# Performance work log

Measured on AMD Instinct MI355X. Metric: run time of the kernel, lower is better.

## Reference

```python
import jax, jax.numpy as jnp
import numpy as np

B, N, M, C, DIN, DIM, SDIM = 4, 65536, 32768, 4, 64, 64, 32


def setup_inputs() -> dict:
    key = jax.random.key(0)
    ks = jax.random.split(key, 8)
    return {
        "last": jax.random.normal(ks[0], (B, N, C, DIN), jnp.float32),
        "sample": jax.random.normal(ks[1], (B, N, C, SDIM), jnp.float32),
        "child_l": jax.random.randint(ks[2], (M,), 0, N),
        "child_r": jax.random.randint(ks[3], (M,), 0, N),
        "child_s": jax.random.randint(ks[4], (M,), 0, N),
        "W_merge": jax.random.normal(ks[5], (2 * DIN, DIM), jnp.float32) / np.float32(np.sqrt(2 * DIN)),
        "b_merge": jnp.zeros((DIM,), jnp.float32),
        "a_merge": jnp.full((1,), 0.25, jnp.float32),
        "W_ms": jax.random.normal(ks[6], (C * SDIM, C * DIM), jnp.float32) / np.float32(np.sqrt(C * SDIM)),
        "b_ms": jnp.zeros((C * DIM,), jnp.float32),
        "a_ms": jnp.full((1,), 0.25, jnp.float32),
        "W_msamp": jax.random.normal(ks[7], (2 * DIM, DIM), jnp.float32) / np.float32(np.sqrt(2 * DIM)),
        "b_msamp": jnp.zeros((DIM,), jnp.float32),
        "a_msamp": jnp.full((1,), 0.25, jnp.float32),
    }


def _prelu(x, a):
    return jnp.where(x >= 0, x, a * x)


def reference(last, sample, child_l, child_r, child_s,
              W_merge, b_merge, a_merge,
              W_ms, b_ms, a_ms,
              W_msamp, b_msamp, a_msamp):
    # gather left/right child embeddings: [B, M, C, DIN] each
    lch = last[:, child_l]
    rch = last[:, child_r]
    x = jnp.concatenate([lch, rch], axis=-1)           # [B, M, C, 2*DIN]
    ans = _prelu(x @ W_merge + b_merge, a_merge)       # [B, M, C, DIM]

    # sampled branch: gather + flatten channel*sample_dim, FC to channel*dim
    s = sample[:, child_s]                             # [B, M, C, SDIM]
    s = s.reshape(s.shape[0], s.shape[1], -1)          # [B, M, C*SDIM]
    s = _prelu(s @ W_ms + b_ms, a_ms)                  # [B, M, C*DIM]
    s = s.reshape(s.shape[0], s.shape[1], ans.shape[2], -1)  # [B, M, C, DIM]

    y = jnp.concatenate([ans, s], axis=-1)             # [B, M, C, 2*DIM]
    out = _prelu(y @ W_msamp + b_msamp, a_msamp)       # [B, M, C, DIM]
    # dropout is identity in eval mode
    return out
```

## Files before the change

### kernel.cpp

```cpp
#include <hip/hip_runtime.h>
#include <hip/hip_bf16.h>

#define B_    4
#define N_TOT 65536
#define M_TOT 32768
#define C_    4
#define DIN_  64
#define DIM_  64
#define SDIM_ 32

typedef __bf16 bf16x8 __attribute__((ext_vector_type(8)));
typedef float  f32x4  __attribute__((ext_vector_type(4)));
typedef bf16x8 bf16x8_a __attribute__((may_alias));
typedef uint2  uint2_a  __attribute__((may_alias));

__device__ __forceinline__ float prelu_f(float x, float a) { return x >= 0.0f ? x : a * x; }

__global__ void prep_weights(const float* __restrict__ Wm,
                             const float* __restrict__ Wms,
                             const float* __restrict__ Wsa,
                             __hip_bfloat16* __restrict__ ws)
{
    int t = blockIdx.x * blockDim.x + threadIdx.x;
    if (t < 8192) {
        int n = t >> 7, k = t & 127;
        ws[t] = __float2bfloat16(Wm[k * 64 + n]);
    } else if (t < 40960) {
        int u = t - 8192; int n = u >> 7, k = u & 127;
        ws[t] = __float2bfloat16(Wms[k * 256 + n]);
    } else if (t < 49152) {
        int u = t - 40960; int n = u >> 7, k = u & 127;
        ws[t] = __float2bfloat16(Wsa[k * 64 + n]);
    }
}

__global__ __launch_bounds__(256, 2) void encoder_fused(
    const float* __restrict__ last,
    const float* __restrict__ sample,
    const int* __restrict__ child_l,
    const int* __restrict__ child_r,
    const int* __restrict__ child_s,
    const __bf16* __restrict__ wt,
    const float* __restrict__ b_merge, const float* __restrict__ a_merge_p,
    const float* __restrict__ b_ms,    const float* __restrict__ a_ms_p,
    const float* __restrict__ b_msamp, const float* __restrict__ a_msamp_p,
    float* __restrict__ out)
{
    __shared__ char lds_raw[4][16384];
    const int tid  = threadIdx.x;
    const int lane = tid & 63;
    const int wid  = tid >> 6;
    char* Y = &lds_raw[wid][0];

    const int group  = blockIdx.x * 4 + wid;
    const int b      = group >> 11;
    const int m_base = (group & 2047) << 4;

    const int g   = lane >> 4;
    const int j15 = lane & 15;

    const float a_merge = *a_merge_p;
    const float a_ms    = *a_ms_p;
    const float a_msamp = *a_msamp_p;

    const __bf16* Wm_t  = wt;
    const __bf16* Wms_t = wt + 8192;
    const __bf16* Wsa_t = wt + 40960;

    bf16x8 wm[4][4];
    f32x4  bm[4];
#pragma unroll
    for (int n = 0; n < 4; ++n) {
        bm[n] = *(const f32x4*)(b_merge + n * 16 + g * 4);
#pragma unroll
        for (int kk = 0; kk < 4; ++kk)
            wm[n][kk] = *(const bf16x8*)(Wm_t + (n * 16 + j15) * 128 + kk * 32 + g * 8);
    }

#pragma unroll
    for (int t = 0; t < 4; ++t) {
        const int node_local = t * 4 + (j15 >> 2);
        const int c  = j15 & 3;
        const int m  = m_base + node_local;
        const int cl = child_l[m];
        const int cr = child_r[m];
        const float* lsrc = last + ((size_t)(b * N_TOT + cl) * C_ + c) * DIN_;
        const float* rsrc = last + ((size_t)(b * N_TOT + cr) * C_ + c) * DIN_;

        bf16x8 xf[4];
#pragma unroll
        for (int kk = 0; kk < 4; ++kk) {
            const int k = kk * 32 + g * 8;
            const float* src = (k < 64) ? (lsrc + k) : (rsrc + (k - 64));
            f32x4 f0 = *(const f32x4*)(src);
            f32x4 f1 = *(const f32x4*)(src + 4);
            bf16x8 v;
            v[0] = (__bf16)f0[0]; v[1] = (__bf16)f0[1]; v[2] = (__bf16)f0[2]; v[3] = (__bf16)f0[3];
            v[4] = (__bf16)f1[0]; v[5] = (__bf16)f1[1]; v[6] = (__bf16)f1[2]; v[7] = (__bf16)f1[3];
            xf[kk] = v;
        }

        const int row = t * 16 + j15;
        const int swz = (row & 7) << 4;
#pragma unroll
        for (int n = 0; n < 4; ++n) {
            f32x4 acc = {0.f, 0.f, 0.f, 0.f};
#pragma unroll
            for (int kk = 0; kk < 4; ++kk)
                acc = __builtin_amdgcn_mfma_f32_16x16x32_bf16(wm[n][kk], xf[kk], acc, 0, 0, 0);
            union { __bf16 h[4]; uint2 u2; } p;
#pragma unroll
            for (int r = 0; r < 4; ++r)
                p.h[r] = (__bf16)prelu_f(acc[r] + bm[n][r], a_merge);
            const int byte = row * 256 + ((n * 32 + g * 8) ^ swz);
            *(uint2_a*)(Y + byte) = p.u2;
        }
    }

    {
        const int m  = m_base + j15;
        const int cs = child_s[m];
        const float* ssrc = sample + (size_t)(b * N_TOT + cs) * 128;
        bf16x8 sf[4];
#pragma unroll
        for (int kk = 0; kk < 4; ++kk) {
            const int k = kk * 32 + g * 8;
            f32x4 f0 = *(const f32x4*)(ssrc + k);
            f32x4 f1 = *(const f32x4*)(ssrc + k + 4);
            bf16x8 v;
            v[0] = (__bf16)f0[0]; v[1] = (__bf16)f0[1]; v[2] = (__bf16)f0[2]; v[3] = (__bf16)f0[3];
            v[4] = (__bf16)f1[0]; v[5] = (__bf16)f1[1]; v[6] = (__bf16)f1[2]; v[7] = (__bf16)f1[3];
            sf[kk] = v;
        }
#pragma unroll
        for (int n2 = 0; n2 < 16; ++n2) {
            f32x4 acc = {0.f, 0.f, 0.f, 0.f};
#pragma unroll
            for (int kk = 0; kk < 4; ++kk) {
                bf16x8 w = *(const bf16x8*)(Wms_t + (n2 * 16 + j15) * 128 + kk * 32 + g * 8);
                acc = __builtin_amdgcn_mfma_f32_16x16x32_bf16(w, sf[kk], acc, 0, 0, 0);
            }
            f32x4 bb = *(const f32x4*)(b_ms + n2 * 16 + g * 4);
            const int f0i = n2 * 16 + g * 4;
            const int row = j15 * 4 + (f0i >> 6);
            const int byte = row * 256 + ((128 + (f0i & 63) * 2) ^ ((row & 7) << 4));
            union { __bf16 h[4]; uint2 u2; } p;
#pragma unroll
            for (int r = 0; r < 4; ++r)
                p.h[r] = (__bf16)prelu_f(acc[r] + bb[r], a_ms);
            *(uint2_a*)(Y + byte) = p.u2;
        }
    }

    bf16x8 wa[4][4];
    f32x4  ba[4];
#pragma unroll
    for (int n = 0; n < 4; ++n) {
        ba[n] = *(const f32x4*)(b_msamp + n * 16 + g * 4);
#pragma unroll
        for (int kk = 0; kk < 4; ++kk)
            wa[n][kk] = *(const bf16x8*)(Wsa_t + (n * 16 + j15) * 128 + kk * 32 + g * 8);
    }

#pragma unroll
    for (int t = 0; t < 4; ++t) {
        const int row = t * 16 + j15;
        const int swz = (row & 7) << 4;
        bf16x8 yf[4];
#pragma unroll
        for (int kk = 0; kk < 4; ++kk) {
            const int byte = row * 256 + ((kk * 64 + g * 16) ^ swz);
            yf[kk] = *(const bf16x8_a*)(Y + byte);
        }
        const int node_local = t * 4 + (j15 >> 2);
        const int c = j15 & 3;
        float* obase = out + (size_t)((b * M_TOT + (m_base + node_local)) * C_ + c) * DIM_;
#pragma unroll
        for (int n = 0; n < 4; ++n) {
            f32x4 acc = {0.f, 0.f, 0.f, 0.f};
#pragma unroll
            for (int kk = 0; kk < 4; ++kk)
                acc = __builtin_amdgcn_mfma_f32_16x16x32_bf16(wa[n][kk], yf[kk], acc, 0, 0, 0);
            f32x4 o;
#pragma unroll
            for (int r = 0; r < 4; ++r)
                o[r] = prelu_f(acc[r] + ba[n][r], a_msamp);
            *(f32x4*)(obase + n * 16 + g * 4) = o;
        }
    }
}

extern "C" void kernel_launch(void* const* d_in, const int* in_sizes, int n_in,
                              void* d_out, int out_size, void* d_ws, size_t ws_size,
                              hipStream_t stream)
{
    const float* last    = (const float*)d_in[0];
    const float* sample  = (const float*)d_in[1];
    const int*   child_l = (const int*)d_in[2];
    const int*   child_r = (const int*)d_in[3];
    const int*   child_s = (const int*)d_in[4];
    const float* W_merge = (const float*)d_in[5];
    const float* b_merge = (const float*)d_in[6];
    const float* a_merge = (const float*)d_in[7];
    const float* W_ms    = (const float*)d_in[8];
    const float* b_ms    = (const float*)d_in[9];
    const float* a_ms    = (const float*)d_in[10];
    const float* W_msamp = (const float*)d_in[11];
    const float* b_msamp = (const float*)d_in[12];
    const float* a_msamp = (const float*)d_in[13];
    float* out = (float*)d_out;

    hipLaunchKernelGGL(prep_weights, dim3(192), dim3(256), 0, stream,
                       W_merge, W_ms, W_msamp, (__hip_bfloat16*)d_ws);

    hipLaunchKernelGGL(encoder_fused, dim3(2048), dim3(256), 0, stream,
                       last, sample, child_l, child_r, child_s,
                       (const __bf16*)d_ws,
                       b_merge, a_merge, b_ms, a_ms, b_msamp, a_msamp, out);
}
```

Before: 162.4 us.

## Prefetch gathers, pass merge outputs via lane shuffles, halve LDS for occupancy

Child indices and the sample row are loaded up front, and the next tile's left/right gathers are double-buffered in registers so they overlap with MFMA work. The merge-branch output now goes to the final GEMM's operands through cross-lane shuffles instead of a round trip through LDS. Only the sampled branch stays in LDS, which halves the LDS footprint and allows launch bounds of 4 blocks per CU. Weights are loaded per use instead of being held in registers, which cuts register pressure at the cost of more L1/L2 weight traffic.

New measurement: 248.2 us. +52.9%, slower.

```diff
diff --git a/kernel.cpp b/kernel.cpp
--- a/kernel.cpp
+++ b/kernel.cpp
@@ -1,20 +1,23 @@
 #include <hip/hip_runtime.h>
 #include <hip/hip_bf16.h>
 
-#define B_    4
 #define N_TOT 65536
 #define M_TOT 32768
-#define C_    4
-#define DIN_  64
-#define DIM_  64
-#define SDIM_ 32
 
 typedef __bf16 bf16x8 __attribute__((ext_vector_type(8)));
 typedef float  f32x4  __attribute__((ext_vector_type(4)));
 typedef bf16x8 bf16x8_a __attribute__((may_alias));
 typedef uint2  uint2_a  __attribute__((may_alias));
 
-__device__ __forceinline__ float prelu_f(float x, float a) { return x >= 0.0f ? x : a * x; }
+__device__ __forceinline__ float prelu_f(float x, float a) { return x >= 0.f ? x : a * x; }
+__device__ __forceinline__ int swzf(int row) { return ((row ^ (row >> 3)) & 7) << 4; }
+
+__device__ __forceinline__ bf16x8 cvt8(f32x4 a, f32x4 b) {
+    bf16x8 v;
+    v[0] = (__bf16)a[0]; v[1] = (__bf16)a[1]; v[2] = (__bf16)a[2]; v[3] = (__bf16)a[3];
+    v[4] = (__bf16)b[0]; v[5] = (__bf16)b[1]; v[6] = (__bf16)b[2]; v[7] = (__bf16)b[3];
+    return v;
+}
 
 __global__ void prep_weights(const float* __restrict__ Wm,
                              const float* __restrict__ Wms,
@@ -34,7 +37,7 @@
     }
 }
 
-__global__ __launch_bounds__(256, 2) void encoder_fused(
+__global__ __launch_bounds__(256, 4) void encoder_fused(
     const float* __restrict__ last,
     const float* __restrict__ sample,
     const int* __restrict__ child_l,
@@ -46,7 +49,7 @@
     const float* __restrict__ b_msamp, const float* __restrict__ a_msamp_p,
     float* __restrict__ out)
 {
-    __shared__ char lds_raw[4][16384];
+    __shared__ char lds_raw[4][8192];
     const int tid  = threadIdx.x;
     const int lane = tid & 63;
     const int wid  = tid >> 6;
@@ -58,6 +61,8 @@
 
     const int g   = lane >> 4;
     const int j15 = lane & 15;
+    const int nl  = j15 >> 2;
+    const int c   = j15 & 3;
 
     const float a_merge = *a_merge_p;
     const float a_ms    = *a_ms_p;
@@ -67,124 +72,134 @@
     const __bf16* Wms_t = wt + 8192;
     const __bf16* Wsa_t = wt + 40960;
 
-    bf16x8 wm[4][4];
-    f32x4  bm[4];
-#pragma unroll
-    for (int n = 0; n < 4; ++n) {
-        bm[n] = *(const f32x4*)(b_merge + n * 16 + g * 4);
-#pragma unroll
-        for (int kk = 0; kk < 4; ++kk)
-            wm[n][kk] = *(const bf16x8*)(Wm_t + (n * 16 + j15) * 128 + kk * 32 + g * 8);
-    }
-
+    int cl[4], cr[4];
 #pragma unroll
     for (int t = 0; t < 4; ++t) {
-        const int node_local = t * 4 + (j15 >> 2);
-        const int c  = j15 & 3;
-        const int m  = m_base + node_local;
-        const int cl = child_l[m];
-        const int cr = child_r[m];
-        const float* lsrc = last + ((size_t)(b * N_TOT + cl) * C_ + c) * DIN_;
-        const float* rsrc = last + ((size_t)(b * N_TOT + cr) * C_ + c) * DIN_;
+        cl[t] = child_l[m_base + t * 4 + nl];
+        cr[t] = child_r[m_base + t * 4 + nl];
+    }
+    const int cs = child_s[m_base + j15];
+
+    const float* ssrc = sample + ((size_t)(b * N_TOT + cs)) * 128;
+    f32x4 sr[8];
+#pragma unroll
+    for (int kk = 0; kk < 4; ++kk) {
+        sr[2 * kk]     = *(const f32x4*)(ssrc + kk * 32 + g * 8);
+        sr[2 * kk + 1] = *(const f32x4*)(ssrc + kk * 32 + g * 8 + 4);
+    }
+
+    f32x4 gr[2][8];
+    {
+        const float* lsrc = last + ((size_t)((b * N_TOT + cl[0]) * 4 + c)) * 64;
+        const float* rsrc = last + ((size_t)((b * N_TOT + cr[0]) * 4 + c)) * 64;
+#pragma unroll
+        for (int kk = 0; kk < 4; ++kk) {
+            const float* src = (kk < 2 ? lsrc + kk * 32 : rsrc + (kk - 2) * 32) + g * 8;
+            gr[0][2 * kk]     = *(const f32x4*)(src);
+            gr[0][2 * kk + 1] = *(const f32x4*)(src + 4);
+        }
+    }
+
+    bf16x8 sf[4];
+#pragma unroll
+    for (int kk = 0; kk < 4; ++kk) sf[kk] = cvt8(sr[2 * kk], sr[2 * kk + 1]);
+#pragma unroll
+    for (int n2 = 0; n2 < 16; ++n2) {
+        f32x4 acc = {0.f, 0.f, 0.f, 0.f};
+#pragma unroll
+        for (int kk = 0; kk < 4; ++kk) {
+            bf16x8 w = *(const bf16x8*)(Wms_t + (n2 * 16 + j15) * 128 + kk * 32 + g * 8);
+            acc = __builtin_amdgcn_mfma_f32_16x16x32_bf16(w, sf[kk], acc, 0, 0, 0);
+        }
+        f32x4 bb = *(const f32x4*)(b_ms + n2 * 16 + g * 4);
+        union { __bf16 h[4]; uint2 u2; } p;
+#pragma unroll
+        for (int r = 0; r < 4; ++r) p.h[r] = (__bf16)prelu_f(acc[r] + bb[r], a_ms);
+        const int row = j15 * 4 + (n2 >> 2);
+        const int d   = (n2 & 3) * 16 + g * 4;
+        *(uint2_a*)(Y + row * 128 + ((2 * d) ^ swzf(row))) = p.u2;
+    }
+
+#pragma unroll
+    for (int t = 0; t < 4; ++t) {
+        if (t < 3) {
+            const float* lsrc = last + ((size_t)((b * N_TOT + cl[t + 1]) * 4 + c)) * 64;
+            const float* rsrc = last + ((size_t)((b * N_TOT + cr[t + 1]) * 4 + c)) * 64;
+#pragma unroll
+            for (int kk = 0; kk < 4; ++kk) {
+                const float* src = (kk < 2 ? lsrc + kk * 32 : rsrc + (kk - 2) * 32) + g * 8;
+                gr[(t + 1) & 1][2 * kk]     = *(const f32x4*)(src);
+                gr[(t + 1) & 1][2 * kk + 1] = *(const f32x4*)(src + 4);
+            }
+        }
 
         bf16x8 xf[4];
 #pragma unroll
-        for (int kk = 0; kk < 4; ++kk) {
-            const int k = kk * 32 + g * 8;
-            const float* src = (k < 64) ? (lsrc + k) : (rsrc + (k - 64));
-            f32x4 f0 = *(const f32x4*)(src);
-            f32x4 f1 = *(const f32x4*)(src + 4);
-            bf16x8 v;
-            v[0] = (__bf16)f0[0]; v[1] = (__bf16)f0[1]; v[2] = (__bf16)f0[2]; v[3] = (__bf16)f0[3];
-            v[4] = (__bf16)f1[0]; v[5] = (__bf16)f1[1]; v[6] = (__bf16)f1[2]; v[7] = (__bf16)f1[3];
-            xf[kk] = v;
-        }
-
-        const int row = t * 16 + j15;
-        const int swz = (row & 7) << 4;
+        for (int kk = 0; kk < 4; ++kk) xf[kk] = cvt8(gr[t & 1][2 * kk], gr[t & 1][2 * kk + 1]);
+
+        uint32_t pnx[4], pny[4];
 #pragma unroll
         for (int n = 0; n < 4; ++n) {
             f32x4 acc = {0.f, 0.f, 0.f, 0.f};
 #pragma unroll
-            for (int kk = 0; kk < 4; ++kk)
-                acc = __builtin_amdgcn_mfma_f32_16x16x32_bf16(wm[n][kk], xf[kk], acc, 0, 0, 0);
-            union { __bf16 h[4]; uint2 u2; } p;
-#pragma unroll
-            for (int r = 0; r < 4; ++r)
-                p.h[r] = (__bf16)prelu_f(acc[r] + bm[n][r], a_merge);
-            const int byte = row * 256 + ((n * 32 + g * 8) ^ swz);
-            *(uint2_a*)(Y + byte) = p.u2;
-        }
-    }
-
-    {
-        const int m  = m_base + j15;
-        const int cs = child_s[m];
-        const float* ssrc = sample + (size_t)(b * N_TOT + cs) * 128;
-        bf16x8 sf[4];
-#pragma unroll
-        for (int kk = 0; kk < 4; ++kk) {
-            const int k = kk * 32 + g * 8;
-            f32x4 f0 = *(const f32x4*)(ssrc + k);
-            f32x4 f1 = *(const f32x4*)(ssrc + k + 4);
-            bf16x8 v;
-            v[0] = (__bf16)f0[0]; v[1] = (__bf16)f0[1]; v[2] = (__bf16)f0[2]; v[3] = (__bf16)f0[3];
-            v[4] = (__bf16)f1[0]; v[5] = (__bf16)f1[1]; v[6] = (__bf16)f1[2]; v[7] = (__bf16)f1[3];
-            sf[kk] = v;
-        }
-#pragma unroll
-        for (int n2 = 0; n2 < 16; ++n2) {
-            f32x4 acc = {0.f, 0.f, 0.f, 0.f};
-#pragma unroll
             for (int kk = 0; kk < 4; ++kk) {
-                bf16x8 w = *(const bf16x8*)(Wms_t + (n2 * 16 + j15) * 128 + kk * 32 + g * 8);
-                acc = __builtin_amdgcn_mfma_f32_16x16x32_bf16(w, sf[kk], acc, 0, 0, 0);
+                bf16x8 w = *(const bf16x8*)(Wm_t + (n * 16 + j15) * 128 + kk * 32 + g * 8);
+                acc = __builtin_amdgcn_mfma_f32_16x16x32_bf16(w, xf[kk], acc, 0, 0, 0);
             }
-            f32x4 bb = *(const f32x4*)(b_ms + n2 * 16 + g * 4);
-            const int f0i = n2 * 16 + g * 4;
-            const int row = j15 * 4 + (f0i >> 6);
-            const int byte = row * 256 + ((128 + (f0i & 63) * 2) ^ ((row & 7) << 4));
-            union { __bf16 h[4]; uint2 u2; } p;
-#pragma unroll
-            for (int r = 0; r < 4; ++r)
-                p.h[r] = (__bf16)prelu_f(acc[r] + bb[r], a_ms);
-            *(uint2_a*)(Y + byte) = p.u2;
-        }
-    }
-
-    bf16x8 wa[4][4];
-    f32x4  ba[4];
-#pragma unroll
-    for (int n = 0; n < 4; ++n) {
-        ba[n] = *(const f32x4*)(b_msamp + n * 16 + g * 4);
-#pragma unroll
-        for (int kk = 0; kk < 4; ++kk)
-            wa[n][kk] = *(const bf16x8*)(Wsa_t + (n * 16 + j15) * 128 + kk * 32 + g * 8);
-    }
-
-#pragma unroll
-    for (int t = 0; t < 4; ++t) {
+            f32x4 bm = *(const f32x4*)(b_merge + n * 16 + g * 4);
+            union { __bf16 h[4]; uint32_t u[2]; } p;
+#pragma unroll
+            for (int r = 0; r < 4; ++r) p.h[r] = (__bf16)prelu_f(acc[r] + bm[r], a_merge);
+            pnx[n] = p.u[0]; pny[n] = p.u[1];
+        }
+
+        const int dlo = (4 - g) & 3;
+        const int dhi = dlo ^ 1;
+        uint32_t lox[2], loy[2], hix[2], hiy[2];
+#pragma unroll
+        for (int d = 0; d < 4; ++d) {
+            const int nsbit = ((g ^ d) >> 1) & 1;
+#pragma unroll
+            for (int kk = 0; kk < 2; ++kk) {
+                uint32_t vx = nsbit ? pnx[2 * kk + 1] : pnx[2 * kk];
+                uint32_t vy = nsbit ? pny[2 * kk + 1] : pny[2 * kk];
+                uint32_t rx = d ? __shfl_xor(vx, d << 4, 64) : vx;
+                uint32_t ry = d ? __shfl_xor(vy, d << 4, 64) : vy;
+                if (d == 0) {
+                    lox[kk] = rx; loy[kk] = ry; hix[kk] = rx; hiy[kk] = ry;
+                } else {
+                    lox[kk] = (dlo == d) ? rx : lox[kk];
+                    loy[kk] = (dlo == d) ? ry : loy[kk];
+                    hix[kk] = (dhi == d) ? rx : hix[kk];
+                    hiy[kk] = (dhi == d) ? ry : hiy[kk];
+                }
+            }
+        }
+        union { uint32_t u[4]; bf16x8_a v; } yf0, yf1;
+        yf0.u[0] = lox[0]; yf0.u[1] = loy[0]; yf0.u[2] = hix[0]; yf0.u[3] = hiy[0];
+        yf1.u[0] = lox[1]; yf1.u[1] = loy[1]; yf1.u[2] = hix[1]; yf1.u[3] = hiy[1];
+
         const int row = t * 16 + j15;
-        const int swz = (row & 7) << 4;
-        bf16x8 yf[4];
-#pragma unroll
-        for (int kk = 0; kk < 4; ++kk) {
-            const int byte = row * 256 + ((kk * 64 + g * 16) ^ swz);
-            yf[kk] = *(const bf16x8_a*)(Y + byte);
-        }
-        const int node_local = t * 4 + (j15 >> 2);
-        const int c = j15 & 3;
-        float* obase = out + (size_t)((b * M_TOT + (m_base + node_local)) * C_ + c) * DIM_;
+        const int sz  = swzf(row);
+        bf16x8 yf2 = *(const bf16x8_a*)(Y + row * 128 + ((16 * g) ^ sz));
+        bf16x8 yf3 = *(const bf16x8_a*)(Y + row * 128 + ((64 + 16 * g) ^ sz));
+
+        float* obase = out + ((size_t)((b * M_TOT + m_base + t * 4 + nl) * 4 + c)) * 64;
 #pragma unroll
         for (int n = 0; n < 4; ++n) {
             f32x4 acc = {0.f, 0.f, 0.f, 0.f};
-#pragma unroll
-            for (int kk = 0; kk < 4; ++kk)
-                acc = __builtin_amdgcn_mfma_f32_16x16x32_bf16(wa[n][kk], yf[kk], acc, 0, 0, 0);
+            bf16x8 w0 = *(const bf16x8*)(Wsa_t + (n * 16 + j15) * 128 + 0 * 32 + g * 8);
+            bf16x8 w1 = *(const bf16x8*)(Wsa_t + (n * 16 + j15) * 128 + 1 * 32 + g * 8);
+            bf16x8 w2 = *(const bf16x8*)(Wsa_t + (n * 16 + j15) * 128 + 2 * 32 + g * 8);
+            bf16x8 w3 = *(const bf16x8*)(Wsa_t + (n * 16 + j15) * 128 + 3 * 32 + g * 8);
+            acc = __builtin_amdgcn_mfma_f32_16x16x32_bf16(w0, yf0.v, acc, 0, 0, 0);
+            acc = __builtin_amdgcn_mfma_f32_16x16x32_bf16(w1, yf1.v, acc, 0, 0, 0);
+            acc = __builtin_amdgcn_mfma_f32_16x16x32_bf16(w2, yf2,   acc, 0, 0, 0);
+            acc = __builtin_amdgcn_mfma_f32_16x16x32_bf16(w3, yf3,   acc, 0, 0, 0);
+            f32x4 ba = *(const f32x4*)(b_msamp + n * 16 + g * 4);
             f32x4 o;
 #pragma unroll
-            for (int r = 0; r < 4; ++r)
-                o[r] = prelu_f(acc[r] + ba[n][r], a_msamp);
+            for (int r = 0; r < 4; ++r) o[r] = prelu_f(acc[r] + ba[r], a_msamp);
             *(f32x4*)(obase + n * 16 + g * 4) = o;
         }
     }
```
